# Performance work log

Hardware: AMD Instinct MI355X
Metric: run time of the kernel (lower is better)

## Reference

```python
import jax, jax.numpy as jnp
import numpy as np

DIM = 2048
NUM_HEADS = 16
NUM_KV_HEADS = 4
HEAD_DIM = DIM // NUM_HEADS  # 128


def apply_rotary_emb(x, freqs_cis):
    # x: [b, s, h, head_dim]; freqs_cis: [s, head_dim//2, 2]
    b, s, h, d = x.shape
    xs = x.reshape(b, s, h, d // 2, 2)
    fc = freqs_cis.reshape(1, s, 1, d // 2, 2)
    real = xs[..., 0] * fc[..., 0] - xs[..., 1] * fc[..., 1]
    imag = xs[..., 1] * fc[..., 0] + xs[..., 0] * fc[..., 1]
    return jnp.stack([real, imag], axis=-1).reshape(b, s, h, d)


def setup_inputs() -> dict:
    key = jax.random.key(0)
    k1, k2, k3, k4 = jax.random.split(key, 4)
    b, s = 2, 2048
    x = jax.random.normal(k1, (b, s, DIM), dtype=jnp.float32)
    freqs_cis = jax.random.uniform(k2, (s, HEAD_DIM // 2, 2), dtype=jnp.float32)
    total_kv_dim = (NUM_HEADS + 2 * NUM_KV_HEADS) * HEAD_DIM  # 3072
    wqkv = jax.random.normal(k3, (total_kv_dim, DIM), dtype=jnp.float32) * (DIM ** -0.5)
    wo = jax.random.normal(k4, (DIM, DIM), dtype=jnp.float32) * (DIM ** -0.5)
    return {"x": x, "freqs_cis": freqs_cis, "wqkv": wqkv, "wo": wo}


def reference(x, freqs_cis, wqkv, wo):
    b, s, _ = x.shape
    kv_size = NUM_KV_HEADS * HEAD_DIM
    qkv = jnp.einsum('bsd,od->bso', x, wqkv)
    xq = qkv[..., :DIM].reshape(b, s, NUM_HEADS, HEAD_DIM)
    xk = qkv[..., DIM:DIM + kv_size].reshape(b, s, NUM_KV_HEADS, HEAD_DIM)
    xv = qkv[..., DIM + kv_size:].reshape(b, s, NUM_KV_HEADS, HEAD_DIM)
    xq = apply_rotary_emb(xq, freqs_cis)
    xk = apply_rotary_emb(xk, freqs_cis)
    # -> [b, h, s, d]
    q = xq.transpose(0, 2, 1, 3)
    k = xk.transpose(0, 2, 1, 3)
    v = xv.transpose(0, 2, 1, 3)
    rep = NUM_HEADS // NUM_KV_HEADS
    k = jnp.repeat(k, rep, axis=1)
    v = jnp.repeat(v, rep, axis=1)
    scale = HEAD_DIM ** -0.5
    scores = jnp.einsum('bhqd,bhkd->bhqk', q, k) * scale
    causal = jnp.tril(jnp.ones((s, s), dtype=bool))
    scores = jnp.where(causal[None, None], scores, jnp.finfo(scores.dtype).min)
    attn = jax.nn.softmax(scores, axis=-1)
    out = jnp.einsum('bhqk,bhkd->bhqd', attn, v)
    out = out.transpose(0, 2, 1, 3).reshape(b, s, DIM)
    return jnp.einsum('bsd,od->bso', out, wo)
```

## Files before the change

kernel.cpp:

```cpp
#include <hip/hip_runtime.h>
#include <stdint.h>

typedef uint16_t u16;
typedef float f32x4 __attribute__((ext_vector_type(4)));
typedef short bf16x8 __attribute__((ext_vector_type(8)));

constexpr int NB = 2, NS = 2048, ND = 2048, NH = 16, NKVH = 4, HDIM = 128;
constexpr int QKVD = 3072;
constexpr int TOK = NB * NS;
constexpr float SM_SCALE = 0.08838834764831845f;
constexpr float LOG2E = 1.4426950408889634f;
constexpr float QK_SCALE = SM_SCALE * LOG2E;

#define WAITVM(N) asm volatile("s_waitcnt vmcnt(" #N ")" ::: "memory")
#define WAITLGKM0 asm volatile("s_waitcnt lgkmcnt(0)" ::: "memory")
#define MEMFENCE asm volatile("" ::: "memory")

__device__ __forceinline__ u16 f2bf(float f) {
  union { float f; uint32_t u; } v; v.f = f;
  return (u16)((v.u + 0x7fffu + ((v.u >> 16) & 1u)) >> 16);
}
__device__ __forceinline__ uint32_t cvt_pk_bf16(float lo, float hi) {
  uint32_t r;
  asm("v_cvt_pk_bf16_f32 %0, %1, %2" : "=v"(r) : "v"(lo), "v"(hi));
  return r;
}

__device__ __forceinline__ void gload_lds16(const void* g, void* l) {
  void* gv = const_cast<void*>(g);
  __builtin_amdgcn_global_load_lds(
      (__attribute__((address_space(1))) void*)gv,
      (__attribute__((address_space(3))) void*)l, 16, 0, 0);
}

__global__ __launch_bounds__(256) void cvt_bf16(const float* __restrict__ src,
                                                u16* __restrict__ dst, int n4) {
  int i = blockIdx.x * 256 + threadIdx.x;
  if (i >= n4) return;
  const float4 v = reinterpret_cast<const float4*>(src)[i];
  union { u16 h[4]; uint2 u; } o;
  o.h[0] = f2bf(v.x); o.h[1] = f2bf(v.y); o.h[2] = f2bf(v.z); o.h[3] = f2bf(v.w);
  reinterpret_cast<uint2*>(dst)[i] = o.u;
}

template <int MODE>
__global__ __launch_bounds__(256, 2)
void gemm_bt(const u16* __restrict__ A, const u16* __restrict__ Bm,
             void* __restrict__ Cv, int M, int N, int K,
             const float* __restrict__ fc, u16* __restrict__ Qb,
             u16* __restrict__ Kb, u16* __restrict__ Vt) {
  __shared__ u16 As[2][128 * 32];
  __shared__ u16 Bs[2][128 * 32];
  const int tid = threadIdx.x;
  const int lane = tid & 63;
  const int wid = tid >> 6;
  const int wr = wid >> 1, wc = wid & 1;
  const int rowA0 = blockIdx.y * 128, colB0 = blockIdx.x * 128;
  const int lr = lane & 15;
  const int lg = lane >> 4;
  const int lk = lg * 8;
  const char* Ab = (const char*)A;
  const char* Bb = (const char*)Bm;
  f32x4 acc[4][4] = {};
  const int nkt = K >> 5;

  auto STAGE = [&](int kt, int buf) {
#pragma unroll
    for (int p = 0; p < 2; ++p) {
      int o = p * 4096 + tid * 16;
      int row = o >> 6, kb = o & 63;
      gload_lds16(Ab + ((size_t)(rowA0 + row) * K + kt * 32) * 2 + kb, (char*)As[buf] + o);
      gload_lds16(Bb + ((size_t)(colB0 + row) * K + kt * 32) * 2 + kb, (char*)Bs[buf] + o);
    }
  };

  STAGE(0, 0);
  for (int kt = 0; kt < nkt; ++kt) {
    const int cur = kt & 1;
    if (kt + 1 < nkt) { STAGE(kt + 1, cur ^ 1); WAITVM(4); }
    else              { WAITVM(0); }
    __builtin_amdgcn_s_barrier();
    MEMFENCE;
    const u16* Ac = As[cur];
    const u16* Bc = Bs[cur];
    bf16x8 af[4], bfr[4];
#pragma unroll
    for (int m = 0; m < 4; ++m)
      af[m] = *(const bf16x8*)&Ac[(wr * 64 + m * 16 + lr) * 32 + lk];
#pragma unroll
    for (int n = 0; n < 4; ++n)
      bfr[n] = *(const bf16x8*)&Bc[(wc * 64 + n * 16 + lr) * 32 + lk];
    __builtin_amdgcn_s_setprio(1);
#pragma unroll
    for (int m = 0; m < 4; ++m)
#pragma unroll
      for (int n = 0; n < 4; ++n)
        acc[m][n] = __builtin_amdgcn_mfma_f32_16x16x32_bf16(af[m], bfr[n], acc[m][n], 0, 0, 0);
    __builtin_amdgcn_s_setprio(0);
    WAITLGKM0;
    __builtin_amdgcn_s_barrier();
    MEMFENCE;
  }

  if (MODE == 0) {
#pragma unroll
    for (int m = 0; m < 4; ++m) {
      int row0 = rowA0 + wr * 64 + m * 16 + lg * 4;
#pragma unroll
      for (int n = 0; n < 4; ++n) {
        int col = colB0 + wc * 64 + n * 16 + lr;
#pragma unroll
        for (int r = 0; r < 4; ++r)
          ((float*)Cv)[(size_t)(row0 + r) * N + col] = acc[m][n][r];
      }
    }
  } else {
    const int colblk = colB0 >> 7;
#pragma unroll
    for (int m = 0; m < 4; ++m) {
      int row0 = rowA0 + wr * 64 + m * 16 + lg * 4;
      int b_ = row0 >> 11;
      int s0 = row0 & 2047;
#pragma unroll
      for (int n = 0; n < 4; ++n) {
        int d = wc * 64 + n * 16 + lr;
        f32x4 v = acc[m][n];
        if (colblk < 20) {
          f32x4 pw;
#pragma unroll
          for (int r = 0; r < 4; ++r) pw[r] = __shfl_xor(v[r], 1, 64);
          int p = d >> 1;
          const bool ev = !(d & 1);
#pragma unroll
          for (int r = 0; r < 4; ++r) {
            int st = s0 + r;
            float c = fc[(st * 64 + p) * 2];
            float sn = fc[(st * 64 + p) * 2 + 1];
            float res = ev ? (v[r] * c - pw[r] * sn) : (v[r] * c + pw[r] * sn);
            if (colblk < 16)
              Qb[((size_t)(b_ * NH + colblk) * NS + st) * HDIM + d] = f2bf(res);
            else
              Kb[((size_t)(b_ * NKVH + (colblk - 16)) * NS + st) * HDIM + d] =
                  f2bf(res * QK_SCALE);
          }
        } else {
          int kv = colblk - 20;
          union { u16 h[4]; uint2 u; } o;
#pragma unroll
          for (int r = 0; r < 4; ++r) o.h[r] = f2bf(v[r]);
          *(uint2*)&Vt[((size_t)(b_ * NKVH + kv) * HDIM + d) * NS + s0] = o.u;
        }
      }
    }
  }
}

__global__ __launch_bounds__(512, 2)
void flash_attn(const u16* __restrict__ Qb, const u16* __restrict__ Kb,
                const u16* __restrict__ Vt, u16* __restrict__ Ob) {
  __shared__ u16 Ks[2][64 * 128];
  __shared__ u16 Vs[2][128 * 64];
  const int idx = blockIdx.x;
  const int grp = idx & 7;
  const int b = grp >> 2, kvh = grp & 3;
  const int rest = idx >> 3;
  const int h = kvh * 4 + (rest & 3);
  const int pair = rest >> 2;
  const int tid = threadIdx.x, lane = tid & 63, w = tid >> 6;
  const int lr = lane & 15, lg = lane >> 4;

  bf16x8 ones;
#pragma unroll
  for (int j = 0; j < 8; ++j) ones[j] = (short)0x3F80;

  const char* Kbase = (const char*)(Kb + (size_t)(b * NKVH + kvh) * NS * HDIM);
  const char* Vbase = (const char*)(Vt + (size_t)(b * NKVH + kvh) * HDIM * NS);

  auto STAGE = [&](int kt, int buf) {
#pragma unroll
    for (int p = 0; p < 2; ++p) {
      int o = p * 8192 + tid * 16;
      int krow = o >> 8, kwb = o & 255;
      gload_lds16(Kbase + (size_t)(kt * 64 + krow) * 256 + (kwb ^ ((krow & 7) << 4)),
                  (char*)Ks[buf] + o);
      int vrow = o >> 7, vwb = o & 127;
      gload_lds16(Vbase + (size_t)vrow * (NS * 2) + kt * 128 + (vwb ^ ((vrow & 7) << 4)),
                  (char*)Vs[buf] + o);
    }
  };

  for (int t = 0; t < 2; ++t) {
    const int qt = t ? (NS / 128 - 1 - pair) : pair;

    bf16x8 aq[4];
    {
      const u16* Qrow = Qb + ((size_t)(b * NH + h) * NS + qt * 128 + w * 16 + lr) * HDIM;
#pragma unroll
      for (int ks = 0; ks < 4; ++ks)
        aq[ks] = *(const bf16x8*)(Qrow + ks * 32 + lg * 8);
    }

    float mrun = -1e30f;
    f32x4 accl = {0.f, 0.f, 0.f, 0.f};
    f32x4 acco[8] = {};

    const int qglob = qt * 128 + w * 16 + lr;
    const int qrow0 = qt * 128 + w * 16 + lg * 4;
    const int wave_min_row = qt * 128 + w * 16;
    const int wave_max_row = wave_min_row + 15;

    const int ktmax = 2 * qt + 1;
    STAGE(0, 0);
    for (int kt = 0; kt <= ktmax; ++kt) {
      const int cur = kt & 1;
      if (kt < ktmax) { STAGE(kt + 1, cur ^ 1); WAITVM(4); }
      else            { WAITVM(0); }
      __builtin_amdgcn_s_barrier();
      MEMFENCE;

      if (kt * 64 <= wave_max_row) {
        const char* Kc = (const char*)Ks[cur];
        const char* Vc = (const char*)Vs[cur];

        f32x4 accs[4] = {};
        __builtin_amdgcn_s_setprio(1);
#pragma unroll
        for (int n = 0; n < 4; ++n) {
          int row = n * 16 + lr;
          int swz = (row & 7) << 4;
#pragma unroll
          for (int ks = 0; ks < 4; ++ks) {
            int cb = (ks * 32 + lg * 8) * 2;
            bf16x8 bk = *(const bf16x8*)(Kc + row * 256 + (cb ^ swz));
            accs[n] = __builtin_amdgcn_mfma_f32_16x16x32_bf16(bk, aq[ks], accs[n], 0, 0, 0);
          }
        }
        __builtin_amdgcn_s_setprio(0);

        if (kt * 64 + 63 > wave_min_row) {
#pragma unroll
          for (int n = 0; n < 4; ++n) {
            int kbase = kt * 64 + n * 16 + lg * 4;
#pragma unroll
            for (int r = 0; r < 4; ++r)
              if (kbase + r > qglob) accs[n][r] = -1e30f;
          }
        }

        float pmax = fmaxf(fmaxf(fmaxf(accs[0][0], accs[0][1]), fmaxf(accs[0][2], accs[0][3])),
                           fmaxf(fmaxf(accs[1][0], accs[1][1]), fmaxf(accs[1][2], accs[1][3])));
        pmax = fmaxf(pmax,
               fmaxf(fmaxf(fmaxf(accs[2][0], accs[2][1]), fmaxf(accs[2][2], accs[2][3])),
                     fmaxf(fmaxf(accs[3][0], accs[3][1]), fmaxf(accs[3][2], accs[3][3]))));
        pmax = fmaxf(pmax, __shfl_xor(pmax, 16, 64));
        pmax = fmaxf(pmax, __shfl_xor(pmax, 32, 64));

        bool ok = (pmax <= mrun + 8.f);
        if (!__all(ok)) {
          float mnew = fmaxf(mrun, pmax);
          float alpha = exp2f(mrun - mnew);
          mrun = mnew;
          float alr[4];
#pragma unroll
          for (int r = 0; r < 4; ++r)
            alr[r] = __shfl(alpha, lg * 4 + r, 64);
#pragma unroll
          for (int r = 0; r < 4; ++r) accl[r] *= alr[r];
#pragma unroll
          for (int n2 = 0; n2 < 8; ++n2)
#pragma unroll
            for (int r = 0; r < 4; ++r) acco[n2][r] *= alr[r];
        }

        uint32_t w0[4], w1[4];
#pragma unroll
        for (int n = 0; n < 4; ++n) {
          float p0 = exp2f(accs[n][0] - mrun);
          float p1 = exp2f(accs[n][1] - mrun);
          float p2 = exp2f(accs[n][2] - mrun);
          float p3 = exp2f(accs[n][3] - mrun);
          w0[n] = cvt_pk_bf16(p0, p1);
          w1[n] = cvt_pk_bf16(p2, p3);
        }

        const int s1 = ((lg & 1) << 5) | lr;
        const int s2 = s1 + 16;
        uint32_t F[4][4];
#pragma unroll
        for (int n = 0; n < 4; ++n) {
          F[n][0] = __shfl((int)w0[n], s1, 64);
          F[n][1] = __shfl((int)w1[n], s1, 64);
          F[n][2] = __shfl((int)w0[n], s2, 64);
          F[n][3] = __shfl((int)w1[n], s2, 64);
        }
        const bool hi = (lg & 2);
        bf16x8 pa[2];
#pragma unroll
        for (int ks = 0; ks < 2; ++ks) {
          union { uint32_t d[4]; bf16x8 v; } u;
#pragma unroll
          for (int j = 0; j < 4; ++j)
            u.d[j] = hi ? F[ks * 2 + 1][j] : F[ks * 2][j];
          pa[ks] = u.v;
        }

        __builtin_amdgcn_s_setprio(1);
#pragma unroll
        for (int ks = 0; ks < 2; ++ks) {
          int cb = (ks * 32 + lg * 8) * 2;
#pragma unroll
          for (int n2 = 0; n2 < 8; ++n2) {
            int d = n2 * 16 + lr;
            bf16x8 bv = *(const bf16x8*)(Vc + d * 128 + (cb ^ ((d & 7) << 4)));
            acco[n2] = __builtin_amdgcn_mfma_f32_16x16x32_bf16(pa[ks], bv, acco[n2], 0, 0, 0);
          }
          accl = __builtin_amdgcn_mfma_f32_16x16x32_bf16(pa[ks], ones, accl, 0, 0, 0);
        }
        __builtin_amdgcn_s_setprio(0);
      }
      WAITLGKM0;
      __builtin_amdgcn_s_barrier();
      MEMFENCE;
    }

#pragma unroll
    for (int n2 = 0; n2 < 8; ++n2) {
      int d = n2 * 16 + lr;
#pragma unroll
      for (int r = 0; r < 4; ++r) {
        int q = qrow0 + r;
        Ob[((size_t)b * NS + q) * ND + h * HDIM + d] = f2bf(acco[n2][r] / accl[r]);
      }
    }
  }
}

extern "C" void kernel_launch(void* const* d_in, const int* in_sizes, int n_in,
                              void* d_out, int out_size, void* d_ws, size_t ws_size,
                              hipStream_t stream) {
  const float* x = (const float*)d_in[0];
  const float* fc = (const float*)d_in[1];
  const float* wqkv = (const float*)d_in[2];
  const float* wo = (const float*)d_in[3];
  float* out = (float*)d_out;
  char* ws = (char*)d_ws;
  size_t off = 0;
  u16* xb = (u16*)(ws + off);    off += (size_t)TOK * ND * 2;
  u16* wqkvb = (u16*)(ws + off); off += (size_t)QKVD * ND * 2;
  u16* wob = (u16*)(ws + off);   off += (size_t)ND * ND * 2;
  u16* Qb = (u16*)(ws + off);    off += (size_t)NB * NH * NS * HDIM * 2;
  u16* Kb = (u16*)(ws + off);    off += (size_t)NB * NKVH * NS * HDIM * 2;
  u16* Vtb = (u16*)(ws + off);   off += (size_t)NB * NKVH * NS * HDIM * 2;
  u16* attnb = (u16*)(ws + off); off += (size_t)TOK * ND * 2;
  (void)ws_size; (void)in_sizes; (void)n_in; (void)out_size;

  cvt_bf16<<<TOK * ND / 4 / 256, 256, 0, stream>>>(x, xb, TOK * ND / 4);
  cvt_bf16<<<QKVD * ND / 4 / 256, 256, 0, stream>>>(wqkv, wqkvb, QKVD * ND / 4);
  cvt_bf16<<<ND * ND / 4 / 256, 256, 0, stream>>>(wo, wob, ND * ND / 4);
  gemm_bt<2><<<dim3(QKVD / 128, TOK / 128), 256, 0, stream>>>(
      xb, wqkvb, nullptr, TOK, QKVD, ND, fc, Qb, Kb, Vtb);
  flash_attn<<<dim3(256), 512, 0, stream>>>(Qb, Kb, Vtb, attnb);
  gemm_bt<0><<<dim3(ND / 128, TOK / 128), 256, 0, stream>>>(
      attnb, wob, out, TOK, ND, ND, nullptr, nullptr, nullptr, nullptr);
}
```

Before: 217.6 us.

## Use 256x256 tiled pipelined GEMM with fused RoPE for QKV projection

Replaces the 128x128 QKV projection GEMM with a dedicated 256x256-tile, 512-thread kernel. It splits each 64-wide K step into two 32-wide LDS halves and interleaves global-to-LDS prefetch with MFMA phases. The RoPE/Q/K/V scatter epilogue is kept per column block. The larger tile raises operand reuse and cuts LDS traffic per flop, but launches only 192 blocks with a large LDS footprint, which can underfill the CUs. The output GEMM is simplified to a non-templated fp32 store kernel.

```diff
diff --git a/kernel.cpp b/kernel.cpp
--- a/kernel.cpp
+++ b/kernel.cpp
@@ -43,12 +43,180 @@
   reinterpret_cast<uint2*>(dst)[i] = o.u;
 }
 
-template <int MODE>
+__global__ __launch_bounds__(512, 2)
+void gemm256_rope(const u16* __restrict__ A, const u16* __restrict__ Bm,
+                  const float* __restrict__ fc, u16* __restrict__ Qb,
+                  u16* __restrict__ Kb, u16* __restrict__ Vt,
+                  int M, int N, int K) {
+  __shared__ u16 As[2][2][256 * 32];
+  __shared__ u16 Bs[2][2][256 * 32];
+  const int tid = threadIdx.x;
+  const int lane = tid & 63;
+  const int wid = tid >> 6;
+  const int wm = wid >> 2;
+  const int wn = wid & 3;
+  const int rowA0 = blockIdx.y * 256, colB0 = blockIdx.x * 256;
+  const int lr = lane & 15, lg = lane >> 4;
+  const char* Ab = (const char*)A;
+  const char* Bb = (const char*)Bm;
+  const int nkt = K >> 6;
+
+  f32x4 acc[8][4] = {};
+
+  auto SA = [&](int kt, int k) {
+#pragma unroll
+    for (int i = 0; i < 2; ++i) {
+      int o = i * 8192 + tid * 16;
+      int r = o >> 6, c = o & 63;
+      gload_lds16(Ab + ((size_t)(rowA0 + r) * K + kt * 64 + k * 32) * 2 + c,
+                  (char*)As[kt & 1][k] + o);
+    }
+  };
+  auto SB = [&](int kt, int k) {
+#pragma unroll
+    for (int i = 0; i < 2; ++i) {
+      int o = i * 8192 + tid * 16;
+      int r = o >> 6, c = o & 63;
+      gload_lds16(Bb + ((size_t)(colB0 + r) * K + kt * 64 + k * 32) * 2 + c,
+                  (char*)Bs[kt & 1][k] + o);
+    }
+  };
+
+  SA(0, 0); SB(0, 0);
+  SA(0, 1); SB(0, 1);
+  SA(1, 0); SB(1, 0);
+  WAITVM(8);
+  __builtin_amdgcn_s_barrier();
+  MEMFENCE;
+
+  for (int t = 0; t < nkt; ++t) {
+    const int d = t & 1;
+    const u16* Ap0 = &As[d][0][0];
+    const u16* Bp0 = &Bs[d][0][0];
+    const u16* Ap1 = &As[d][1][0];
+    const u16* Bp1 = &Bs[d][1][0];
+    bf16x8 af[4], bf[4];
+
+#pragma unroll
+    for (int m = 0; m < 4; ++m)
+      af[m] = *(const bf16x8*)&Ap0[(wm * 128 + m * 16 + lr) * 32 + lg * 8];
+#pragma unroll
+    for (int n = 0; n < 4; ++n)
+      bf[n] = *(const bf16x8*)&Bp0[(wn * 64 + n * 16 + lr) * 32 + lg * 8];
+    if (t + 1 < nkt) SA(t + 1, 1);
+    __builtin_amdgcn_s_barrier();
+    MEMFENCE;
+    __builtin_amdgcn_s_setprio(1);
+#pragma unroll
+    for (int m = 0; m < 4; ++m)
+#pragma unroll
+      for (int n = 0; n < 4; ++n)
+        acc[m][n] = __builtin_amdgcn_mfma_f32_16x16x32_bf16(af[m], bf[n], acc[m][n], 0, 0, 0);
+    __builtin_amdgcn_s_setprio(0);
+    MEMFENCE;
+    __builtin_amdgcn_s_barrier();
+    MEMFENCE;
+
+#pragma unroll
+    for (int m = 0; m < 4; ++m)
+      af[m] = *(const bf16x8*)&Ap0[(wm * 128 + (m + 4) * 16 + lr) * 32 + lg * 8];
+    if (t + 1 < nkt) SB(t + 1, 1);
+    __builtin_amdgcn_s_barrier();
+    MEMFENCE;
+    __builtin_amdgcn_s_setprio(1);
+#pragma unroll
+    for (int m = 0; m < 4; ++m)
+#pragma unroll
+      for (int n = 0; n < 4; ++n)
+        acc[m + 4][n] = __builtin_amdgcn_mfma_f32_16x16x32_bf16(af[m], bf[n], acc[m + 4][n], 0, 0, 0);
+    __builtin_amdgcn_s_setprio(0);
+    if (t + 1 < nkt) WAITVM(8); else WAITVM(0);
+    __builtin_amdgcn_s_barrier();
+    MEMFENCE;
+
+#pragma unroll
+    for (int m = 0; m < 4; ++m)
+      af[m] = *(const bf16x8*)&Ap1[(wm * 128 + m * 16 + lr) * 32 + lg * 8];
+#pragma unroll
+    for (int n = 0; n < 4; ++n)
+      bf[n] = *(const bf16x8*)&Bp1[(wn * 64 + n * 16 + lr) * 32 + lg * 8];
+    if (t + 2 < nkt) SA(t + 2, 0);
+    __builtin_amdgcn_s_barrier();
+    MEMFENCE;
+    __builtin_amdgcn_s_setprio(1);
+#pragma unroll
+    for (int m = 0; m < 4; ++m)
+#pragma unroll
+      for (int n = 0; n < 4; ++n)
+        acc[m][n] = __builtin_amdgcn_mfma_f32_16x16x32_bf16(af[m], bf[n], acc[m][n], 0, 0, 0);
+    __builtin_amdgcn_s_setprio(0);
+    MEMFENCE;
+    __builtin_amdgcn_s_barrier();
+    MEMFENCE;
+
+#pragma unroll
+    for (int m = 0; m < 4; ++m)
+      af[m] = *(const bf16x8*)&Ap1[(wm * 128 + (m + 4) * 16 + lr) * 32 + lg * 8];
+    if (t + 2 < nkt) SB(t + 2, 0);
+    __builtin_amdgcn_s_barrier();
+    MEMFENCE;
+    __builtin_amdgcn_s_setprio(1);
+#pragma unroll
+    for (int m = 0; m < 4; ++m)
+#pragma unroll
+      for (int n = 0; n < 4; ++n)
+        acc[m + 4][n] = __builtin_amdgcn_mfma_f32_16x16x32_bf16(af[m], bf[n], acc[m + 4][n], 0, 0, 0);
+    __builtin_amdgcn_s_setprio(0);
+    if (t + 1 < nkt) {
+      if (t + 2 < nkt) WAITVM(8); else WAITVM(4);
+    }
+    __builtin_amdgcn_s_barrier();
+    MEMFENCE;
+  }
+
+#pragma unroll
+  for (int m = 0; m < 8; ++m) {
+    int row0 = rowA0 + wm * 128 + m * 16 + lg * 4;
+    int b_ = row0 >> 11;
+    int s0 = row0 & 2047;
+#pragma unroll
+    for (int n = 0; n < 4; ++n) {
+      int col = colB0 + wn * 64 + n * 16 + lr;
+      int colblk = col >> 7;
+      int dd = col & 127;
+      f32x4 v = acc[m][n];
+      if (colblk < 20) {
+        f32x4 pw;
+#pragma unroll
+        for (int r = 0; r < 4; ++r) pw[r] = __shfl_xor(v[r], 1, 64);
+        int p = dd >> 1;
+        const bool ev = !(dd & 1);
+#pragma unroll
+        for (int r = 0; r < 4; ++r) {
+          int st = s0 + r;
+          float c = fc[(st * 64 + p) * 2];
+          float sn = fc[(st * 64 + p) * 2 + 1];
+          float res = ev ? (v[r] * c - pw[r] * sn) : (v[r] * c + pw[r] * sn);
+          if (colblk < 16)
+            Qb[((size_t)(b_ * NH + colblk) * NS + st) * HDIM + dd] = f2bf(res);
+          else
+            Kb[((size_t)(b_ * NKVH + (colblk - 16)) * NS + st) * HDIM + dd] =
+                f2bf(res * QK_SCALE);
+        }
+      } else {
+        int kv = colblk - 20;
+        union { u16 h[4]; uint2 u; } o;
+#pragma unroll
+        for (int r = 0; r < 4; ++r) o.h[r] = f2bf(v[r]);
+        *(uint2*)&Vt[((size_t)(b_ * NKVH + kv) * HDIM + dd) * NS + s0] = o.u;
+      }
+    }
+  }
+}
+
 __global__ __launch_bounds__(256, 2)
 void gemm_bt(const u16* __restrict__ A, const u16* __restrict__ Bm,
-             void* __restrict__ Cv, int M, int N, int K,
-             const float* __restrict__ fc, u16* __restrict__ Qb,
-             u16* __restrict__ Kb, u16* __restrict__ Vt) {
+             float* __restrict__ C, int M, int N, int K) {
   __shared__ u16 As[2][128 * 32];
   __shared__ u16 Bs[2][128 * 32];
   const int tid = threadIdx.x;
@@ -101,56 +269,15 @@
     __builtin_amdgcn_s_barrier();
     MEMFENCE;
   }
-
-  if (MODE == 0) {
-#pragma unroll
-    for (int m = 0; m < 4; ++m) {
-      int row0 = rowA0 + wr * 64 + m * 16 + lg * 4;
-#pragma unroll
-      for (int n = 0; n < 4; ++n) {
-        int col = colB0 + wc * 64 + n * 16 + lr;
-#pragma unroll
-        for (int r = 0; r < 4; ++r)
-          ((float*)Cv)[(size_t)(row0 + r) * N + col] = acc[m][n][r];
-      }
-    }
-  } else {
-    const int colblk = colB0 >> 7;
-#pragma unroll
-    for (int m = 0; m < 4; ++m) {
-      int row0 = rowA0 + wr * 64 + m * 16 + lg * 4;
-      int b_ = row0 >> 11;
-      int s0 = row0 & 2047;
-#pragma unroll
-      for (int n = 0; n < 4; ++n) {
-        int d = wc * 64 + n * 16 + lr;
-        f32x4 v = acc[m][n];
-        if (colblk < 20) {
-          f32x4 pw;
-#pragma unroll
-          for (int r = 0; r < 4; ++r) pw[r] = __shfl_xor(v[r], 1, 64);
-          int p = d >> 1;
-          const bool ev = !(d & 1);
-#pragma unroll
-          for (int r = 0; r < 4; ++r) {
-            int st = s0 + r;
-            float c = fc[(st * 64 + p) * 2];
-            float sn = fc[(st * 64 + p) * 2 + 1];
-            float res = ev ? (v[r] * c - pw[r] * sn) : (v[r] * c + pw[r] * sn);
-            if (colblk < 16)
-              Qb[((size_t)(b_ * NH + colblk) * NS + st) * HDIM + d] = f2bf(res);
-            else
-              Kb[((size_t)(b_ * NKVH + (colblk - 16)) * NS + st) * HDIM + d] =
-                  f2bf(res * QK_SCALE);
-          }
-        } else {
-          int kv = colblk - 20;
-          union { u16 h[4]; uint2 u; } o;
-#pragma unroll
-          for (int r = 0; r < 4; ++r) o.h[r] = f2bf(v[r]);
-          *(uint2*)&Vt[((size_t)(b_ * NKVH + kv) * HDIM + d) * NS + s0] = o.u;
-        }
-      }
+#pragma unroll
+  for (int m = 0; m < 4; ++m) {
+    int row0 = rowA0 + wr * 64 + m * 16 + lg * 4;
+#pragma unroll
+    for (int n = 0; n < 4; ++n) {
+      int col = colB0 + wc * 64 + n * 16 + lr;
+#pragma unroll
+      for (int r = 0; r < 4; ++r)
+        C[(size_t)(row0 + r) * N + col] = acc[m][n][r];
     }
   }
 }
@@ -357,9 +484,9 @@
   cvt_bf16<<<TOK * ND / 4 / 256, 256, 0, stream>>>(x, xb, TOK * ND / 4);
   cvt_bf16<<<QKVD * ND / 4 / 256, 256, 0, stream>>>(wqkv, wqkvb, QKVD * ND / 4);
   cvt_bf16<<<ND * ND / 4 / 256, 256, 0, stream>>>(wo, wob, ND * ND / 4);
-  gemm_bt<2><<<dim3(QKVD / 128, TOK / 128), 256, 0, stream>>>(
-      xb, wqkvb, nullptr, TOK, QKVD, ND, fc, Qb, Kb, Vtb);
+  gemm256_rope<<<dim3(QKVD / 256, TOK / 256), 512, 0, stream>>>(
+      xb, wqkvb, fc, Qb, Kb, Vtb, TOK, QKVD, ND);
   flash_attn<<<dim3(256), 512, 0, stream>>>(Qb, Kb, Vtb, attnb);
-  gemm_bt<0><<<dim3(ND / 128, TOK / 128), 256, 0, stream>>>(
-      attnb, wob, out, TOK, ND, ND, nullptr, nullptr, nullptr, nullptr);
-}
+  gemm_bt<<<dim3(ND / 128, TOK / 128), 256, 0, stream>>>(
+      attnb, wob, out, TOK, ND, ND);
+}
```

New measurement: 229.8 us. +5.6%, slower.

## Split attention KV tiles across wave halves, shrink query tiles, fuse conversions

Applied to the files above, without the earlier changes.

Flash attention now uses 64-row query tiles with 512 blocks. The 8 waves split as 4 query groups times 2 key halves, each half handling 32 keys of every 64-key tile. The two partial softmax states (O, l, m) are merged through LDS at the end. This is meant to double block-level parallelism and cut causal-diagonal waste. The three fp32-to-bf16 conversion launches are also fused into one kernel. In exchange it adds an LDS merge, an extra barrier per tile, and more K/V reloads across the extra blocks.

```diff
diff --git a/kernel.cpp b/kernel.cpp
--- a/kernel.cpp
+++ b/kernel.cpp
@@ -33,14 +33,21 @@
       (__attribute__((address_space(3))) void*)l, 16, 0, 0);
 }
 
-__global__ __launch_bounds__(256) void cvt_bf16(const float* __restrict__ src,
-                                                u16* __restrict__ dst, int n4) {
+__global__ __launch_bounds__(256)
+void cvt3(const float* __restrict__ x, const float* __restrict__ wq,
+          const float* __restrict__ wo, u16* __restrict__ xb,
+          u16* __restrict__ wqb, u16* __restrict__ wob) {
+  constexpr int N1 = TOK * ND / 4, N2 = QKVD * ND / 4, N3 = ND * ND / 4;
   int i = blockIdx.x * 256 + threadIdx.x;
-  if (i >= n4) return;
-  const float4 v = reinterpret_cast<const float4*>(src)[i];
+  const float* src; u16* dst; int j;
+  if (i < N1)              { src = x;  dst = xb;  j = i; }
+  else if (i < N1 + N2)    { src = wq; dst = wqb; j = i - N1; }
+  else if (i < N1 + N2 + N3){ src = wo; dst = wob; j = i - N1 - N2; }
+  else return;
+  const float4 v = reinterpret_cast<const float4*>(src)[j];
   union { u16 h[4]; uint2 u; } o;
   o.h[0] = f2bf(v.x); o.h[1] = f2bf(v.y); o.h[2] = f2bf(v.z); o.h[3] = f2bf(v.w);
-  reinterpret_cast<uint2*>(dst)[i] = o.u;
+  reinterpret_cast<uint2*>(dst)[j] = o.u;
 }
 
 template <int MODE>
@@ -158,8 +165,7 @@
 __global__ __launch_bounds__(512, 2)
 void flash_attn(const u16* __restrict__ Qb, const u16* __restrict__ Kb,
                 const u16* __restrict__ Vt, u16* __restrict__ Ob) {
-  __shared__ u16 Ks[2][64 * 128];
-  __shared__ u16 Vs[2][128 * 64];
+  __shared__ char LDS[65536];
   const int idx = blockIdx.x;
   const int grp = idx & 7;
   const int b = grp >> 2, kvh = grp & 3;
@@ -168,6 +174,7 @@
   const int pair = rest >> 2;
   const int tid = threadIdx.x, lane = tid & 63, w = tid >> 6;
   const int lr = lane & 15, lg = lane >> 4;
+  const int qh = w & 3, khalf = w >> 2;
 
   bf16x8 ones;
 #pragma unroll
@@ -182,19 +189,26 @@
       int o = p * 8192 + tid * 16;
       int krow = o >> 8, kwb = o & 255;
       gload_lds16(Kbase + (size_t)(kt * 64 + krow) * 256 + (kwb ^ ((krow & 7) << 4)),
-                  (char*)Ks[buf] + o);
+                  LDS + buf * 16384 + o);
       int vrow = o >> 7, vwb = o & 127;
       gload_lds16(Vbase + (size_t)vrow * (NS * 2) + kt * 128 + (vwb ^ ((vrow & 7) << 4)),
-                  (char*)Vs[buf] + o);
+                  LDS + 32768 + buf * 16384 + o);
     }
   };
 
+  float* scrO = (float*)LDS;
+  float* scrL = (float*)(LDS + 32768);
+  float* scrM = scrL + 64;
+
   for (int t = 0; t < 2; ++t) {
-    const int qt = t ? (NS / 128 - 1 - pair) : pair;
+    const int qtile = t ? (31 - pair) : pair;
+    const int base = qtile * 64 + qh * 16;
+    const int qglob = base + lr;
+    const int qmax = base + 15;
 
     bf16x8 aq[4];
     {
-      const u16* Qrow = Qb + ((size_t)(b * NH + h) * NS + qt * 128 + w * 16 + lr) * HDIM;
+      const u16* Qrow = Qb + ((size_t)(b * NH + h) * NS + base + lr) * HDIM;
 #pragma unroll
       for (int ks = 0; ks < 4; ++ks)
         aq[ks] = *(const bf16x8*)(Qrow + ks * 32 + lg * 8);
@@ -204,12 +218,7 @@
     f32x4 accl = {0.f, 0.f, 0.f, 0.f};
     f32x4 acco[8] = {};
 
-    const int qglob = qt * 128 + w * 16 + lr;
-    const int qrow0 = qt * 128 + w * 16 + lg * 4;
-    const int wave_min_row = qt * 128 + w * 16;
-    const int wave_max_row = wave_min_row + 15;
-
-    const int ktmax = 2 * qt + 1;
+    const int ktmax = qtile;
     STAGE(0, 0);
     for (int kt = 0; kt <= ktmax; ++kt) {
       const int cur = kt & 1;
@@ -218,15 +227,16 @@
       __builtin_amdgcn_s_barrier();
       MEMFENCE;
 
-      if (kt * 64 <= wave_max_row) {
-        const char* Kc = (const char*)Ks[cur];
-        const char* Vc = (const char*)Vs[cur];
-
-        f32x4 accs[4] = {};
+      const int kslice0 = kt * 64 + khalf * 32;
+      if (kslice0 <= qmax) {
+        const char* Kc = LDS + cur * 16384;
+        const char* Vc = LDS + 32768 + cur * 16384;
+
+        f32x4 accs[2] = {};
         __builtin_amdgcn_s_setprio(1);
 #pragma unroll
-        for (int n = 0; n < 4; ++n) {
-          int row = n * 16 + lr;
+        for (int n = 0; n < 2; ++n) {
+          int row = khalf * 32 + n * 16 + lr;
           int swz = (row & 7) << 4;
 #pragma unroll
           for (int ks = 0; ks < 4; ++ks) {
@@ -237,21 +247,18 @@
         }
         __builtin_amdgcn_s_setprio(0);
 
-        if (kt * 64 + 63 > wave_min_row) {
-#pragma unroll
-          for (int n = 0; n < 4; ++n) {
-            int kbase = kt * 64 + n * 16 + lg * 4;
+        if (kslice0 + 31 > base) {
+#pragma unroll
+          for (int n = 0; n < 2; ++n) {
+            int kb = kslice0 + n * 16 + lg * 4;
 #pragma unroll
             for (int r = 0; r < 4; ++r)
-              if (kbase + r > qglob) accs[n][r] = -1e30f;
+              if (kb + r > qglob) accs[n][r] = -1e30f;
           }
         }
 
         float pmax = fmaxf(fmaxf(fmaxf(accs[0][0], accs[0][1]), fmaxf(accs[0][2], accs[0][3])),
                            fmaxf(fmaxf(accs[1][0], accs[1][1]), fmaxf(accs[1][2], accs[1][3])));
-        pmax = fmaxf(pmax,
-               fmaxf(fmaxf(fmaxf(accs[2][0], accs[2][1]), fmaxf(accs[2][2], accs[2][3])),
-                     fmaxf(fmaxf(accs[3][0], accs[3][1]), fmaxf(accs[3][2], accs[3][3]))));
         pmax = fmaxf(pmax, __shfl_xor(pmax, 16, 64));
         pmax = fmaxf(pmax, __shfl_xor(pmax, 32, 64));
 
@@ -272,49 +279,39 @@
             for (int r = 0; r < 4; ++r) acco[n2][r] *= alr[r];
         }
 
-        uint32_t w0[4], w1[4];
-#pragma unroll
-        for (int n = 0; n < 4; ++n) {
-          float p0 = exp2f(accs[n][0] - mrun);
-          float p1 = exp2f(accs[n][1] - mrun);
-          float p2 = exp2f(accs[n][2] - mrun);
-          float p3 = exp2f(accs[n][3] - mrun);
-          w0[n] = cvt_pk_bf16(p0, p1);
-          w1[n] = cvt_pk_bf16(p2, p3);
+        uint32_t w0[2], w1[2];
+#pragma unroll
+        for (int n = 0; n < 2; ++n) {
+          w0[n] = cvt_pk_bf16(exp2f(accs[n][0] - mrun), exp2f(accs[n][1] - mrun));
+          w1[n] = cvt_pk_bf16(exp2f(accs[n][2] - mrun), exp2f(accs[n][3] - mrun));
         }
 
         const int s1 = ((lg & 1) << 5) | lr;
         const int s2 = s1 + 16;
-        uint32_t F[4][4];
-#pragma unroll
-        for (int n = 0; n < 4; ++n) {
-          F[n][0] = __shfl((int)w0[n], s1, 64);
-          F[n][1] = __shfl((int)w1[n], s1, 64);
-          F[n][2] = __shfl((int)w0[n], s2, 64);
-          F[n][3] = __shfl((int)w1[n], s2, 64);
-        }
-        const bool hi = (lg & 2);
-        bf16x8 pa[2];
-#pragma unroll
-        for (int ks = 0; ks < 2; ++ks) {
+        uint32_t F0[4], F1[4];
+        F0[0] = __shfl((int)w0[0], s1, 64); F0[1] = __shfl((int)w1[0], s1, 64);
+        F0[2] = __shfl((int)w0[0], s2, 64); F0[3] = __shfl((int)w1[0], s2, 64);
+        F1[0] = __shfl((int)w0[1], s1, 64); F1[1] = __shfl((int)w1[1], s1, 64);
+        F1[2] = __shfl((int)w0[1], s2, 64); F1[3] = __shfl((int)w1[1], s2, 64);
+        const bool hi = (lg >> 1);
+        bf16x8 pa;
+        {
           union { uint32_t d[4]; bf16x8 v; } u;
 #pragma unroll
-          for (int j = 0; j < 4; ++j)
-            u.d[j] = hi ? F[ks * 2 + 1][j] : F[ks * 2][j];
-          pa[ks] = u.v;
+          for (int j = 0; j < 4; ++j) u.d[j] = hi ? F1[j] : F0[j];
+          pa = u.v;
         }
 
         __builtin_amdgcn_s_setprio(1);
-#pragma unroll
-        for (int ks = 0; ks < 2; ++ks) {
-          int cb = (ks * 32 + lg * 8) * 2;
+        {
+          int cb = (khalf * 32 + lg * 8) * 2;
 #pragma unroll
           for (int n2 = 0; n2 < 8; ++n2) {
             int d = n2 * 16 + lr;
             bf16x8 bv = *(const bf16x8*)(Vc + d * 128 + (cb ^ ((d & 7) << 4)));
-            acco[n2] = __builtin_amdgcn_mfma_f32_16x16x32_bf16(pa[ks], bv, acco[n2], 0, 0, 0);
+            acco[n2] = __builtin_amdgcn_mfma_f32_16x16x32_bf16(pa, bv, acco[n2], 0, 0, 0);
           }
-          accl = __builtin_amdgcn_mfma_f32_16x16x32_bf16(pa[ks], ones, accl, 0, 0, 0);
+          accl = __builtin_amdgcn_mfma_f32_16x16x32_bf16(pa, ones, accl, 0, 0, 0);
         }
         __builtin_amdgcn_s_setprio(0);
       }
@@ -323,15 +320,42 @@
       MEMFENCE;
     }
 
-#pragma unroll
-    for (int n2 = 0; n2 < 8; ++n2) {
-      int d = n2 * 16 + lr;
+    if (khalf == 1) {
+#pragma unroll
+      for (int n2 = 0; n2 < 8; ++n2)
+#pragma unroll
+        for (int r = 0; r < 4; ++r)
+          scrO[qh * 2048 + (lg * 4 + r) * 128 + n2 * 16 + lr] = acco[n2][r];
+      if (lr == 0) {
+#pragma unroll
+        for (int r = 0; r < 4; ++r)
+          scrL[qh * 16 + lg * 4 + r] = accl[r];
+      }
+      if (lg == 0) scrM[qh * 16 + lr] = mrun;
+    }
+    WAITLGKM0;
+    __builtin_amdgcn_s_barrier();
+    MEMFENCE;
+    if (khalf == 0) {
 #pragma unroll
       for (int r = 0; r < 4; ++r) {
-        int q = qrow0 + r;
-        Ob[((size_t)b * NS + q) * ND + h * HDIM + d] = f2bf(acco[n2][r] / accl[r]);
-      }
-    }
+        int q = lg * 4 + r;
+        float ma = __shfl(mrun, q, 64);
+        float mb = scrM[qh * 16 + q];
+        float mt = fmaxf(ma, mb);
+        float sa = exp2f(ma - mt), sb = exp2f(mb - mt);
+        float lb = scrL[qh * 16 + q];
+        float inv = 1.0f / (accl[r] * sa + lb * sb);
+#pragma unroll
+        for (int n2 = 0; n2 < 8; ++n2) {
+          float ob = scrO[qh * 2048 + q * 128 + n2 * 16 + lr];
+          float o = (acco[n2][r] * sa + ob * sb) * inv;
+          Ob[((size_t)b * NS + base + q) * ND + h * HDIM + n2 * 16 + lr] = f2bf(o);
+        }
+      }
+    }
+    __builtin_amdgcn_s_barrier();
+    MEMFENCE;
   }
 }
 
@@ -354,12 +378,11 @@
   u16* attnb = (u16*)(ws + off); off += (size_t)TOK * ND * 2;
   (void)ws_size; (void)in_sizes; (void)n_in; (void)out_size;
 
-  cvt_bf16<<<TOK * ND / 4 / 256, 256, 0, stream>>>(x, xb, TOK * ND / 4);
-  cvt_bf16<<<QKVD * ND / 4 / 256, 256, 0, stream>>>(wqkv, wqkvb, QKVD * ND / 4);
-  cvt_bf16<<<ND * ND / 4 / 256, 256, 0, stream>>>(wo, wob, ND * ND / 4);
+  constexpr int CVTN = (TOK * ND + QKVD * ND + ND * ND) / 4;
+  cvt3<<<CVTN / 256, 256, 0, stream>>>(x, wqkv, wo, xb, wqkvb, wob);
   gemm_bt<2><<<dim3(QKVD / 128, TOK / 128), 256, 0, stream>>>(
       xb, wqkvb, nullptr, TOK, QKVD, ND, fc, Qb, Kb, Vtb);
-  flash_attn<<<dim3(256), 512, 0, stream>>>(Qb, Kb, Vtb, attnb);
+  flash_attn<<<dim3(512), 512, 0, stream>>>(Qb, Kb, Vtb, attnb);
   gemm_bt<0><<<dim3(ND / 128, TOK / 128), 256, 0, stream>>>(
       attnb, wob, out, TOK, ND, ND, nullptr, nullptr, nullptr, nullptr);
 }
```

Measured after the change: 231.1 us. +6.2%, slower.
